# Optimization experiments

Hardware: AMD Instinct MI355X
Metric: run time of the kernel (lower is better)

The kernel has to match this reference:

```python
import jax, jax.numpy as jnp
import numpy as np

N, M, D = 65536, 1024, 2

def setup_inputs() -> dict:
    key = jax.random.key(0)
    k1, k2, k3, k4 = jax.random.split(key, 4)
    sample = jax.random.normal(k1, (N, D), dtype=jnp.float32)
    mu = jax.random.uniform(k2, (M, D), dtype=jnp.float32)
    A = jax.random.normal(k3, (M, D, D), dtype=jnp.float32)
    w = jax.random.normal(k4, (M, 1), dtype=jnp.float32)
    return {"sample": sample, "mu": mu, "A": A, "w": w}


def reference(sample, mu, A, w):
    # Covariance-like precision matrices: gamma_j = A_j A_j^T / 2, shape [M, D, D]
    gamma = jnp.matmul(A, jnp.swapaxes(A, 1, 2)) / 2.0
    # Hand-rolled 2x2 determinants (matches covariances_determinants)
    dets = gamma[:, 0, 0] * gamma[:, 1, 1] - gamma[:, 0, 1] * gamma[:, 1, 0]  # [M]
    # log of the scalar factor in front of each Gaussian (weights_log)
    log_w = jax.nn.log_softmax(w, axis=0)[:, 0] + 0.5 * jnp.log(dets)  # [M]
    # Pairwise Mahalanobis quadratic form q_ij = (x_i - mu_j)^T gamma_j (x_i - mu_j)
    diff = sample[:, None, :] - mu[None, :, :]  # [N, M, D]
    q = jnp.einsum('nmd,mde,nme->nm', diff, gamma, diff)  # [N, M]
    # 'lse' mode of kernel_product: log sum_j exp(log_w_j - q_ij)
    ll = jax.scipy.special.logsumexp(log_w[None, :] - q, axis=1)  # [N]
    return ll[:, None]
```

## Files before the change

kernel.cpp:

```cpp
#include <hip/hip_runtime.h>
#include <math.h>

#define LOG2E 1.4426950408889634f
#define LN2   0.6931471805599453f

typedef float v2f __attribute__((ext_vector_type(2)));

__device__ __forceinline__ float fast_exp2(float x) {
#if __has_builtin(__builtin_amdgcn_exp2f)
    return __builtin_amdgcn_exp2f(x);
#else
    return exp2f(x);
#endif
}

__global__ __launch_bounds__(512, 4) void gm_fused(
        const float* __restrict__ sample,
        const float* __restrict__ mu,
        const float* __restrict__ A,
        const float* __restrict__ w,
        float* __restrict__ out) {
    __shared__ float COEF[6][1024];
    __shared__ float RED[128][65];
    __shared__ float PART[128][5];
    __shared__ float red8[8];

    const int tid  = threadIdx.x;
    const int lane = tid & 63;
    const int wid  = tid >> 6;

    const float2 wv = ((const float2*)w)[tid];

    float v = fmaxf(wv.x, wv.y);
    #pragma unroll
    for (int o = 32; o; o >>= 1) v = fmaxf(v, __shfl_xor(v, o));
    if (lane == 0) red8[wid] = v;
    __syncthreads();
    float wmax = red8[0];
    #pragma unroll
    for (int k = 1; k < 8; k++) wmax = fmaxf(wmax, red8[k]);
    __syncthreads();

    v = expf(wv.x - wmax) + expf(wv.y - wmax);
    #pragma unroll
    for (int o = 32; o; o >>= 1) v += __shfl_xor(v, o);
    if (lane == 0) red8[wid] = v;
    __syncthreads();
    float sumew = 0.f;
    #pragma unroll
    for (int k = 0; k < 8; k++) sumew += red8[k];
    const float lse = wmax + logf(sumew);
    __syncthreads();

    float lw2[2], G00[2], G2[2], G11[2], MX[2], MY[2];
    const float wj[2] = {wv.x, wv.y};
    #pragma unroll
    for (int k = 0; k < 2; k++) {
        const int j = 2 * tid + k;
        const float4 a = ((const float4*)A)[j];
        const float g00 = 0.5f * (a.x*a.x + a.y*a.y);
        const float g01 = 0.5f * (a.x*a.z + a.y*a.w);
        const float g11 = 0.5f * (a.z*a.z + a.w*a.w);
        const float det = g00*g11 - g01*g01;
        lw2[k] = ((wj[k] - lse) + 0.5f * logf(det)) * LOG2E;
        G00[k] = g00 * LOG2E;
        G2[k]  = 2.f * g01 * LOG2E;
        G11[k] = g11 * LOG2E;
        const float2 m = ((const float2*)mu)[j];
        MX[k] = m.x; MY[k] = m.y;
    }

    v = fmaxf(lw2[0], lw2[1]);
    #pragma unroll
    for (int o = 32; o; o >>= 1) v = fmaxf(v, __shfl_xor(v, o));
    if (lane == 0) red8[wid] = v;
    __syncthreads();
    float Lmax = red8[0];
    #pragma unroll
    for (int k = 1; k < 8; k++) Lmax = fmaxf(Lmax, red8[k]);

    #pragma unroll
    for (int k = 0; k < 2; k++) {
        const int j = 2 * tid + k;
        const float mx = MX[k], my = MY[k];
        COEF[0][j] = lw2[k] - (G00[k]*mx*mx + G2[k]*mx*my + G11[k]*my*my) - Lmax;
        COEF[1][j] = 2.f*G00[k]*mx + G2[k]*my;
        COEF[2][j] = G2[k]*mx + 2.f*G11[k]*my;
        COEF[3][j] = -G00[k];
        COEF[4][j] = -G2[k];
        COEF[5][j] = -G11[k];
    }
    __syncthreads();

    v2f C0[8], C1[8], C2[8], D0[8], D1[8], D2[8];
    #pragma unroll
    for (int k = 0; k < 8; k++) {
        const int j = 128*k + lane;
        C0[k] = (v2f){COEF[0][j], COEF[0][j+64]};
        C1[k] = (v2f){COEF[1][j], COEF[1][j+64]};
        C2[k] = (v2f){COEF[2][j], COEF[2][j+64]};
        D0[k] = (v2f){COEF[3][j], COEF[3][j+64]};
        D1[k] = (v2f){COEF[4][j], COEF[4][j+64]};
        D2[k] = (v2f){COEF[5][j], COEF[5][j+64]};
    }

    const int ls0 = wid * 16;
    const int sbu = __builtin_amdgcn_readfirstlane(blockIdx.x * 128 + ls0);

    for (int s = 0; s < 16; ++s) {
        const float2 xy = ((const float2*)sample)[sbu + s];
        const v2f Xv = {xy.x, xy.x}, Yv = {xy.y, xy.y};

        v2f sv = {0.f, 0.f};
        #pragma unroll
        for (int k = 0; k < 8; k++) {
            v2f i1 = __builtin_elementwise_fma(D0[k], Xv, C1[k]);
            i1     = __builtin_elementwise_fma(D1[k], Yv, i1);
            v2f i2 = __builtin_elementwise_fma(D2[k], Yv, C2[k]);
            v2f t  = __builtin_elementwise_fma(i1, Xv, C0[k]);
            t      = __builtin_elementwise_fma(i2, Yv, t);
            sv.x += fast_exp2(t.x);
            sv.y += fast_exp2(t.y);
        }
        RED[ls0 + s][lane] = sv.x + sv.y;
    }
    __syncthreads();

    {
        const int r = tid >> 2, c = tid & 3;
        const float* row = &RED[r][c * 16];
        float p = 0.f;
        #pragma unroll
        for (int i = 0; i < 16; i++) p += row[i];
        PART[r][c] = p;
    }
    __syncthreads();

    if (tid < 128) {
        const float st = (PART[tid][0] + PART[tid][1])
                       + (PART[tid][2] + PART[tid][3]);
        const int si = blockIdx.x * 128 + tid;
        float ll;
        if (st >= 1e-30f) {
            ll = LN2 * (Lmax + log2f(st));
        } else {
            const float2 xy = ((const float2*)sample)[si];
            const float x = xy.x, y = xy.y;
            float m = -3e38f;
            for (int j = 0; j < 1024; j++) {
                float i1 = fmaf(COEF[3][j], x, COEF[1][j]);
                i1 = fmaf(COEF[4][j], y, i1);
                float i2 = fmaf(COEF[5][j], y, COEF[2][j]);
                float t = fmaf(i1, x, COEF[0][j]);
                t = fmaf(i2, y, t);
                m = fmaxf(m, t);
            }
            float ss = 0.f;
            for (int j = 0; j < 1024; j++) {
                float i1 = fmaf(COEF[3][j], x, COEF[1][j]);
                i1 = fmaf(COEF[4][j], y, i1);
                float i2 = fmaf(COEF[5][j], y, COEF[2][j]);
                float t = fmaf(i1, x, COEF[0][j]);
                t = fmaf(i2, y, t);
                ss += fast_exp2(t - m);
            }
            ll = LN2 * (Lmax + m + log2f(ss));
        }
        out[si] = ll;
    }
}

extern "C" void kernel_launch(void* const* d_in, const int* in_sizes, int n_in,
                              void* d_out, int out_size, void* d_ws, size_t ws_size,
                              hipStream_t stream) {
    const float* sample = (const float*)d_in[0];
    const float* mu     = (const float*)d_in[1];
    const float* A      = (const float*)d_in[2];
    const float* w      = (const float*)d_in[3];
    float* out = (float*)d_out;

    const int N = in_sizes[0] / 2;

    gm_fused<<<N / 128, 512, 0, stream>>>(sample, mu, A, w, out);
}
```

Baseline: 19.58 us.

## Split components across wave pairs and alias LDS to raise occupancy

Each block now handles 64 samples instead of 128, and each pair of waves splits the 1024 components in half. This halves the per-thread coefficient registers. The COEF and RED shared buffers are aliased into one LDS region so more blocks fit per CU, and the launch bound asks for 6 blocks. The rare underflow fallback now recomputes the coefficients from global memory because COEF is overwritten. In exchange, the per-block prologue (softmax, coefficient setup) is repeated across twice as many blocks, and an extra barrier is added.

```diff
diff --git a/kernel.cpp b/kernel.cpp
--- a/kernel.cpp
+++ b/kernel.cpp
@@ -14,15 +14,16 @@
 #endif
 }
 
-__global__ __launch_bounds__(512, 4) void gm_fused(
+__global__ __launch_bounds__(512, 6) void gm_fused(
         const float* __restrict__ sample,
         const float* __restrict__ mu,
         const float* __restrict__ A,
         const float* __restrict__ w,
         float* __restrict__ out) {
-    __shared__ float COEF[6][1024];
-    __shared__ float RED[128][65];
-    __shared__ float PART[128][5];
+    __shared__ __align__(16) char LBUF[36096];
+    float (*COEF)[1024] = (float (*)[1024])LBUF;
+    float (*RED)[132]   = (float (*)[132])LBUF;
+    float (*PART)[9]    = (float (*)[9])(LBUF + 64*132*4);
     __shared__ float red8[8];
 
     const int tid  = threadIdx.x;
@@ -92,10 +93,12 @@
     }
     __syncthreads();
 
-    v2f C0[8], C1[8], C2[8], D0[8], D1[8], D2[8];
+    const int g = wid >> 1;
+    const int h = wid & 1;
+    v2f C0[4], C1[4], C2[4], D0[4], D1[4], D2[4];
     #pragma unroll
-    for (int k = 0; k < 8; k++) {
-        const int j = 128*k + lane;
+    for (int k = 0; k < 4; k++) {
+        const int j = h*512 + 128*k + lane;
         C0[k] = (v2f){COEF[0][j], COEF[0][j+64]};
         C1[k] = (v2f){COEF[1][j], COEF[1][j+64]};
         C2[k] = (v2f){COEF[2][j], COEF[2][j+64]};
@@ -103,17 +106,19 @@
         D1[k] = (v2f){COEF[4][j], COEF[4][j+64]};
         D2[k] = (v2f){COEF[5][j], COEF[5][j+64]};
     }
+    __syncthreads();
 
-    const int ls0 = wid * 16;
-    const int sbu = __builtin_amdgcn_readfirstlane(blockIdx.x * 128 + ls0);
+    const int ls0 = g * 16;
+    const int sbu = __builtin_amdgcn_readfirstlane(blockIdx.x * 64 + ls0);
 
+    #pragma unroll 4
     for (int s = 0; s < 16; ++s) {
         const float2 xy = ((const float2*)sample)[sbu + s];
         const v2f Xv = {xy.x, xy.x}, Yv = {xy.y, xy.y};
 
         v2f sv = {0.f, 0.f};
         #pragma unroll
-        for (int k = 0; k < 8; k++) {
+        for (int k = 0; k < 4; k++) {
             v2f i1 = __builtin_elementwise_fma(D0[k], Xv, C1[k]);
             i1     = __builtin_elementwise_fma(D1[k], Yv, i1);
             v2f i2 = __builtin_elementwise_fma(D2[k], Yv, C2[k]);
@@ -122,12 +127,12 @@
             sv.x += fast_exp2(t.x);
             sv.y += fast_exp2(t.y);
         }
-        RED[ls0 + s][lane] = sv.x + sv.y;
+        RED[ls0 + s][h*64 + lane] = sv.x + sv.y;
     }
     __syncthreads();
 
     {
-        const int r = tid >> 2, c = tid & 3;
+        const int r = tid >> 3, c = tid & 7;
         const float* row = &RED[r][c * 16];
         float p = 0.f;
         #pragma unroll
@@ -136,33 +141,36 @@
     }
     __syncthreads();
 
-    if (tid < 128) {
-        const float st = (PART[tid][0] + PART[tid][1])
-                       + (PART[tid][2] + PART[tid][3]);
-        const int si = blockIdx.x * 128 + tid;
+    if (tid < 64) {
+        float st = 0.f;
+        #pragma unroll
+        for (int c = 0; c < 8; c++) st += PART[tid][c];
+        const int si = blockIdx.x * 64 + tid;
         float ll;
         if (st >= 1e-30f) {
             ll = LN2 * (Lmax + log2f(st));
         } else {
             const float2 xy = ((const float2*)sample)[si];
             const float x = xy.x, y = xy.y;
-            float m = -3e38f;
-            for (int j = 0; j < 1024; j++) {
-                float i1 = fmaf(COEF[3][j], x, COEF[1][j]);
-                i1 = fmaf(COEF[4][j], y, i1);
-                float i2 = fmaf(COEF[5][j], y, COEF[2][j]);
-                float t = fmaf(i1, x, COEF[0][j]);
-                t = fmaf(i2, y, t);
-                m = fmaxf(m, t);
-            }
-            float ss = 0.f;
-            for (int j = 0; j < 1024; j++) {
-                float i1 = fmaf(COEF[3][j], x, COEF[1][j]);
-                i1 = fmaf(COEF[4][j], y, i1);
-                float i2 = fmaf(COEF[5][j], y, COEF[2][j]);
-                float t = fmaf(i1, x, COEF[0][j]);
-                t = fmaf(i2, y, t);
-                ss += fast_exp2(t - m);
+            float m = -3e38f, ss = 0.f;
+            for (int pass = 0; pass < 2; pass++) {
+                float acc = -3e38f;
+                if (pass) acc = 0.f;
+                for (int j = 0; j < 1024; j++) {
+                    const float4 a = ((const float4*)A)[j];
+                    const float g00 = 0.5f * (a.x*a.x + a.y*a.y);
+                    const float g01 = 0.5f * (a.x*a.z + a.y*a.w);
+                    const float g11 = 0.5f * (a.z*a.z + a.w*a.w);
+                    const float det = g00*g11 - g01*g01;
+                    const float lw2j = ((w[j] - lse) + 0.5f * logf(det)) * LOG2E;
+                    const float2 mm = ((const float2*)mu)[j];
+                    const float dx = x - mm.x, dy = y - mm.y;
+                    const float q = (g00*dx*dx + 2.f*g01*dx*dy + g11*dy*dy) * LOG2E;
+                    const float t = lw2j - q - Lmax;
+                    if (pass == 0) acc = fmaxf(acc, t);
+                    else           acc += fast_exp2(t - m);
+                }
+                if (pass == 0) m = acc; else ss = acc;
             }
             ll = LN2 * (Lmax + m + log2f(ss));
         }
@@ -181,5 +189,5 @@
 
     const int N = in_sizes[0] / 2;
 
-    gm_fused<<<N / 128, 512, 0, stream>>>(sample, mu, A, w, out);
+    gm_fused<<<N / 64, 512, 0, stream>>>(sample, mu, A, w, out);
 }
```

After: 21.42 us. +9.4%, slower.
